# Kernel optimization log

Measured on AMD Instinct MI355X. Metric: run time of the kernel, lower is better.

Reference implementation:

```python
import jax, jax.numpy as jnp
import numpy as np

KERNEL_MUL = 2.0
KERNEL_NUM = 5


def setup_inputs() -> dict:
    key = jax.random.key(0)
    k1, k2 = jax.random.split(key)
    B, Ns, Nt, K = 4, 2048, 2048, 32
    source = jax.random.normal(k1, (B, Ns, K), dtype=jnp.float32)
    target = jax.random.normal(k2, (B, Nt, K), dtype=jnp.float32)
    return {"source": source, "target": target}


def _mmd_rbf(source, target):
    # source: [B, Ns, K], target: [B, Nt, K]
    Ns = source.shape[1]
    Nt = target.shape[1]
    n_samples = Ns + Nt
    total = jnp.concatenate([source, target], axis=1)  # [B, N, K]
    # Pairwise squared L2 via Gram trick (avoids [B, N, N, K] broadcast tensor)
    sq = jnp.sum(total * total, axis=-1)  # [B, N]
    gram = jnp.einsum('bik,bjk->bij', total, total)  # [B, N, N]
    L2 = sq[:, :, None] + sq[:, None, :] - 2.0 * gram  # [B, N, N]
    # Multi-bandwidth RBF kernel sum
    bw = jnp.sum(L2, axis=(1, 2), keepdims=True) / (n_samples ** 2 - n_samples + 1e-8)  # [B,1,1]
    bw = bw / (KERNEL_MUL ** (KERNEL_NUM // 2))
    # Small fixed loop over bandwidths; accumulate to avoid [K_num, B, N, N] stack.
    kernel = jnp.zeros_like(L2)
    for i in range(KERNEL_NUM):
        kernel = kernel + jnp.exp(-L2 / (bw * (KERNEL_MUL ** i)) + 1e-8)
    # Quadrant means
    N = Ns
    XX = kernel[:, :N, :N].mean(axis=(1, 2))
    YY = kernel[:, N:, N:].mean(axis=(1, 2))
    XY = kernel[:, :N, N:].mean(axis=(1, 2))
    YX = kernel[:, N:, :N].mean(axis=(1, 2))
    return XX + YY - XY - YX  # [B]


def reference(source, target):
    return _mmd_rbf(source, target)
```

## Files before the change

### kernel.cpp

```cpp
#include <hip/hip_runtime.h>
#include <hip/hip_bf16.h>


#define NPTS 4096
#define HALF 2048
#define KDIM 32
#define T3   128
#define NTB3 32
#define NPAIR3 528
#define GRIDX 128
#define SPREAD 64

#define WS_SQ    0
#define WS_PART  65536
#define WS_QUAD  82432
#define WS_COEF  90640
#define WS_FRAG  98304
#define WS_NEED  (98304 + 4 * NPTS * 128)

typedef __attribute__((ext_vector_type(8))) short short8v;
typedef __attribute__((ext_vector_type(4))) float f32x4;

__device__ __forceinline__ float fast_exp2(float x) {
#if __has_builtin(__builtin_amdgcn_exp2f)
  return __builtin_amdgcn_exp2f(x);
#else
  return exp2f(x);
#endif
}

__device__ __forceinline__ unsigned int bf16_rne(float x) {
  unsigned int u = __float_as_uint(x);
  return (u + 0x7fffu + ((u >> 16) & 1u)) >> 16;
}

__device__ __forceinline__ const float* point_ptr(const float* __restrict__ src,
                                                  const float* __restrict__ tgt,
                                                  int b, int p) {
  return (p < HALF) ? src + ((size_t)b * HALF + p) * KDIM
                    : tgt + ((size_t)b * HALF + (p - HALF)) * KDIM;
}

__global__ void mmd_pass1(const float* __restrict__ src, const float* __restrict__ tgt,
                          float* __restrict__ sqArr, double* __restrict__ part1,
                          double* __restrict__ quadbuf,
                          unsigned char* __restrict__ frags, int preFlag) {
  const int b = blockIdx.y;
  const int p = blockIdx.x * 256 + threadIdx.x;

  if (blockIdx.x == 0)
    quadbuf[b * 4 * SPREAD + threadIdx.x] = 0.0;

  const float* __restrict__ xp = point_ptr(src, tgt, b, p);
  float x[KDIM];
#pragma unroll
  for (int q = 0; q < 8; ++q) {
    float4 v = reinterpret_cast<const float4*>(xp)[q];
    x[4*q+0] = v.x; x[4*q+1] = v.y; x[4*q+2] = v.z; x[4*q+3] = v.w;
  }
  float s0 = 0.f, s1 = 0.f, s2 = 0.f, s3 = 0.f;
#pragma unroll
  for (int q = 0; q < 8; ++q) {
    s0 = fmaf(x[4*q+0], x[4*q+0], s0);
    s1 = fmaf(x[4*q+1], x[4*q+1], s1);
    s2 = fmaf(x[4*q+2], x[4*q+2], s2);
    s3 = fmaf(x[4*q+3], x[4*q+3], s3);
  }
  float sq = (s0 + s1) + (s2 + s3);
  sqArr[(size_t)b * NPTS + p] = sq;

  if (preFlag) {
    unsigned int hw[16], lw[16];
#pragma unroll
    for (int e = 0; e < 16; ++e) {
      const float xa = x[2*e], xb = x[2*e+1];
      const unsigned int ha = bf16_rne(xa);
      const unsigned int la = bf16_rne(xa - __uint_as_float(ha << 16));
      const unsigned int hb = bf16_rne(xb);
      const unsigned int lb = bf16_rne(xb - __uint_as_float(hb << 16));
      hw[e] = ha | (hb << 16);
      lw[e] = la | (lb << 16);
    }
    uint4* dst = reinterpret_cast<uint4*>(frags + (size_t)(b * NPTS + p) * 128);
#pragma unroll
    for (int c = 0; c < 4; ++c)
      dst[c] = make_uint4(hw[4*c], hw[4*c+1], hw[4*c+2], hw[4*c+3]);
#pragma unroll
    for (int c = 0; c < 4; ++c)
      dst[4 + c] = make_uint4(lw[4*c], lw[4*c+1], lw[4*c+2], lw[4*c+3]);
  }

  __shared__ float lx[256][KDIM + 1];
  __shared__ float part[8][KDIM];
  __shared__ float sqpart[4];

#pragma unroll
  for (int k = 0; k < KDIM; ++k) lx[threadIdx.x][k] = x[k];

  float w = sq;
#pragma unroll
  for (int off = 32; off > 0; off >>= 1) w += __shfl_down(w, off, 64);
  if ((threadIdx.x & 63) == 0) sqpart[threadIdx.x >> 6] = w;
  __syncthreads();

  const int k = threadIdx.x & 31, g = threadIdx.x >> 5;
  float ps = 0.f;
#pragma unroll 8
  for (int r = 0; r < 32; ++r) ps += lx[g * 32 + r][k];
  part[g][k] = ps;
  __syncthreads();

  double* slot = part1 + ((size_t)b * 16 + blockIdx.x) * 33;
  if (threadIdx.x < 32) {
    float tot = 0.f;
#pragma unroll
    for (int gg = 0; gg < 8; ++gg) tot += part[gg][threadIdx.x];
    slot[1 + threadIdx.x] = (double)tot;
  }
  if (threadIdx.x == 63)
    slot[0] = (double)(sqpart[0] + sqpart[1] + sqpart[2] + sqpart[3]);
}

__global__ void mmd_pass2(const double* __restrict__ part1, float* __restrict__ coef) {
  const int b = threadIdx.x >> 6;
  const int lane = threadIdx.x & 63;
  __shared__ double red[4][33];
  if (lane < 33) {
    double s = 0.0;
    for (int blk = 0; blk < 16; ++blk) s += part1[((size_t)b * 16 + blk) * 33 + lane];
    red[b][lane] = s;
  }
  __syncthreads();
  if (lane == 0) {
    double ssq = red[b][0], s2 = 0.0;
    for (int k = 1; k <= 32; ++k) s2 += red[b][k] * red[b][k];
    const double N = (double)NPTS;
    double bw = (2.0 * N * ssq - 2.0 * s2) / (N * N - N + 1e-8);
    bw *= 0.25;
    coef[b] = (float)(-1.4426950408889634 / (bw * 16.0));
  }
}

__device__ __forceinline__ short8v lds_frag(const unsigned char* base, int p,
                                            int half, int lk) {
  const int slot = (half * 4 + lk) ^ (p & 7);
  return *reinterpret_cast<const short8v*>(base + p * 128 + slot * 16);
}

template <bool PRE>
__global__ void __launch_bounds__(512, 4)
mmd_pass3(const float* __restrict__ src, const float* __restrict__ tgt,
          const float* __restrict__ sqArr, const float* __restrict__ coef,
          const unsigned char* __restrict__ frags,
          double* __restrict__ quadbuf) {
  const int bid = blockIdx.x;
  const int b = blockIdx.y;
  const int tid = threadIdx.x;
  const int lane = tid & 63;
  const int w = tid >> 6;
  const int lm = lane & 15;
  const int lk = lane >> 4;
  const int wr = w & 3;
  const int wc = w >> 2;

  __shared__ __align__(16) unsigned char fragA[2][T3 * 128];
  __shared__ __align__(16) unsigned char fragB[2][T3 * 128];
  __shared__ __align__(16) float s_sqA[2][T3];
  __shared__ __align__(16) float s_sqB[2][T3];
  __shared__ double wsum[2][8];

  const float nc4 = coef[b];
  const float m2nc = -2.0f * nc4;
  const float* __restrict__ sqG = sqArr + (size_t)b * NPTS;
  const uint4* __restrict__ gfr =
      reinterpret_cast<const uint4*>(frags) + (size_t)b * NPTS * 8;

  const int npair = (bid + 4 * GRIDX < NPAIR3) ? 5 : 4;

  int bxA[5], byA[5];
#pragma unroll
  for (int it = 0; it < 5; ++it) {
    const int pi = bid + it * GRIDX;
    int y = (int)((sqrtf((float)(8 * pi + 1)) - 1.0f) * 0.5f);
    while ((y + 1) * (y + 2) / 2 <= pi) ++y;
    while (y * (y + 1) / 2 > pi) --y;
    byA[it] = y; bxA[it] = pi - y * (y + 1) / 2;
  }

  {
    const int bx = bxA[0], by = byA[0];
    if constexpr (PRE) {
#pragma unroll
      for (int i = 0; i < 2; ++i) {
        const int g = tid + i * 512;
        const int p = g >> 3, s = g & 7;
        const int d = p * 8 + (s ^ (p & 7));
        reinterpret_cast<uint4*>(fragA[0])[d] = gfr[(size_t)bx * 1024 + g];
        reinterpret_cast<uint4*>(fragB[0])[d] = gfr[(size_t)by * 1024 + g];
      }
    } else {
      if (tid < 256) {
        const int pt = tid & 127;
        const bool isB = tid >= 128;
        const float* fp = point_ptr(src, tgt, b, (isB ? by : bx) * T3 + pt);
        unsigned int hw[16], lw[16];
#pragma unroll
        for (int e = 0; e < 16; ++e) {
          const float xa = fp[2*e], xb = fp[2*e+1];
          const unsigned int ha = bf16_rne(xa);
          const unsigned int la = bf16_rne(xa - __uint_as_float(ha << 16));
          const unsigned int hb = bf16_rne(xb);
          const unsigned int lb = bf16_rne(xb - __uint_as_float(hb << 16));
          hw[e] = ha | (hb << 16);
          lw[e] = la | (lb << 16);
        }
        uint4* dst = reinterpret_cast<uint4*>((isB ? fragB[0] : fragA[0]) + pt * 128);
#pragma unroll
        for (int s = 0; s < 8; ++s) {
          const unsigned int* s4 = (s < 4) ? &hw[s * 4] : &lw[(s - 4) * 4];
          dst[s ^ (pt & 7)] = make_uint4(s4[0], s4[1], s4[2], s4[3]);
        }
      }
    }
    if (tid < 128) s_sqA[0][tid] = sqG[bx * T3 + tid];
    else if (tid < 256) s_sqB[0][tid - 128] = sqG[by * T3 + (tid - 128)];
  }
  __syncthreads();

  for (int it = 0; it < npair; ++it) {
    const int c = it & 1;
    const int bx = bxA[it], by = byA[it];

    uint4 va[2], vb[2];
    float nsqa = 0.f, nsqb = 0.f;
    const bool havenext = (it + 1 < npair);
    if (havenext) {
      const int nbx = bxA[it + 1], nby = byA[it + 1];
      if constexpr (PRE) {
#pragma unroll
        for (int i = 0; i < 2; ++i) {
          const int g = tid + i * 512;
          va[i] = gfr[(size_t)nbx * 1024 + g];
          vb[i] = gfr[(size_t)nby * 1024 + g];
        }
      }
      if (tid < 128) nsqa = sqG[nbx * T3 + tid];
      else if (tid < 256) nsqb = sqG[nby * T3 + (tid - 128)];
    }

    const unsigned char* fA = fragA[c];
    const unsigned char* fB = fragB[c];

    short8v Bh[4], Bl[4];
    float sjn[4];
#pragma unroll
    for (int cg = 0; cg < 4; ++cg) {
      const int p = wc * 64 + cg * 16 + lm;
      Bh[cg] = lds_frag(fB, p, 0, lk);
      Bl[cg] = lds_frag(fB, p, 1, lk);
      sjn[cg] = s_sqB[c][p] * nc4;
    }

    double accd = 0.0;
#pragma unroll
    for (int rg = 0; rg < 2; ++rg) {
      const int pa = wr * 32 + rg * 16 + lm;
      const short8v Ah = lds_frag(fA, pa, 0, lk);
      const short8v Al = lds_frag(fA, pa, 1, lk);
      const float4 sqi4 = *reinterpret_cast<const float4*>(
          &s_sqA[c][wr * 32 + rg * 16 + lk * 4]);
      const float sin_[4] = {sqi4.x * nc4, sqi4.y * nc4, sqi4.z * nc4, sqi4.w * nc4};
#pragma unroll
      for (int cg = 0; cg < 4; ++cg) {
        f32x4 accP = {0.f, 0.f, 0.f, 0.f};
        f32x4 accQ = {0.f, 0.f, 0.f, 0.f};
        accP = __builtin_amdgcn_mfma_f32_16x16x32_bf16(Ah, Bh[cg], accP, 0, 0, 0);
        accQ = __builtin_amdgcn_mfma_f32_16x16x32_bf16(Ah, Bl[cg], accQ, 0, 0, 0);
        accP = __builtin_amdgcn_mfma_f32_16x16x32_bf16(Al, Bl[cg], accP, 0, 0, 0);
        accQ = __builtin_amdgcn_mfma_f32_16x16x32_bf16(Al, Bh[cg], accQ, 0, 0, 0);
        float rs = 0.f;
#pragma unroll
        for (int reg = 0; reg < 4; ++reg) {
          const float dot = accP[reg] + accQ[reg];
          const float arg = fmaf(dot, m2nc, sin_[reg] + sjn[cg]);
          float e = fast_exp2(arg);
          float s = e;
          e *= e; s += e;
          e *= e; s += e;
          e *= e; s += e;
          e *= e; s += e;
          rs += s;
        }
        accd += (double)rs;
      }
    }

#pragma unroll
    for (int off = 32; off > 0; off >>= 1) accd += __shfl_down(accd, off, 64);
    if (lane == 0) wsum[c][w] = accd;

    if (havenext) {
      if constexpr (PRE) {
#pragma unroll
        for (int i = 0; i < 2; ++i) {
          const int g = tid + i * 512;
          const int p = g >> 3, s = g & 7;
          const int d = p * 8 + (s ^ (p & 7));
          reinterpret_cast<uint4*>(fragA[c ^ 1])[d] = va[i];
          reinterpret_cast<uint4*>(fragB[c ^ 1])[d] = vb[i];
        }
      } else {
        const int nbx = bxA[it + 1], nby = byA[it + 1];
        if (tid < 256) {
          const int pt = tid & 127;
          const bool isB = tid >= 128;
          const float* fp = point_ptr(src, tgt, b, (isB ? nby : nbx) * T3 + pt);
          unsigned int hw[16], lw[16];
#pragma unroll
          for (int e = 0; e < 16; ++e) {
            const float xa = fp[2*e], xb = fp[2*e+1];
            const unsigned int ha = bf16_rne(xa);
            const unsigned int la = bf16_rne(xa - __uint_as_float(ha << 16));
            const unsigned int hb = bf16_rne(xb);
            const unsigned int lb = bf16_rne(xb - __uint_as_float(hb << 16));
            hw[e] = ha | (hb << 16);
            lw[e] = la | (lb << 16);
          }
          uint4* dst = reinterpret_cast<uint4*>(
              (isB ? fragB[c ^ 1] : fragA[c ^ 1]) + pt * 128);
#pragma unroll
          for (int s = 0; s < 8; ++s) {
            const unsigned int* s4 = (s < 4) ? &hw[s * 4] : &lw[(s - 4) * 4];
            dst[s ^ (pt & 7)] = make_uint4(s4[0], s4[1], s4[2], s4[3]);
          }
        }
      }
      if (tid < 128) s_sqA[c ^ 1][tid] = nsqa;
      else if (tid < 256) s_sqB[c ^ 1][tid - 128] = nsqb;
    }

    __syncthreads();

    if (tid == 0) {
      double tot = 0.0;
#pragma unroll
      for (int ww = 0; ww < 8; ++ww) tot += wsum[c][ww];
      const int rh = (bx >= NTB3 / 2) ? 1 : 0;
      const int ch = (by >= NTB3 / 2) ? 1 : 0;
      const int q  = (rh << 1) | ch;
      const int qT = (ch << 1) | rh;
      const int slot = (bx + by * NTB3) & (SPREAD - 1);
      atomicAdd(&quadbuf[(((b << 2) | q) * SPREAD) + slot], tot);
      if (bx != by)
        atomicAdd(&quadbuf[(((b << 2) | qT) * SPREAD) + slot], tot);
    }
  }
}

__global__ void mmd_pass4(const double* __restrict__ quadbuf, float* __restrict__ out) {
  const int tid = threadIdx.x;
  const int qq = tid >> 6, i = tid & 63;
  __shared__ double wsum[4];
  const double inv = 1.0 / ((double)HALF * (double)HALF);
  for (int b = 0; b < 4; ++b) {
    double v = quadbuf[((b << 2) | qq) * SPREAD + i];
    double sv = (qq == 0 || qq == 3) ? v : -v;
#pragma unroll
    for (int off = 32; off > 0; off >>= 1) sv += __shfl_down(sv, off, 64);
    if ((tid & 63) == 0) wsum[qq] = sv;
    __syncthreads();
    if (tid == 0) out[b] = (float)((wsum[0] + wsum[1] + wsum[2] + wsum[3]) * inv);
    __syncthreads();
  }
}

extern "C" void kernel_launch(void* const* d_in, const int* in_sizes, int n_in,
                              void* d_out, int out_size, void* d_ws, size_t ws_size,
                              hipStream_t stream) {
  const float* src = (const float*)d_in[0];
  const float* tgt = (const float*)d_in[1];
  float* out = (float*)d_out;

  char* ws = (char*)d_ws;
  float*         sqArr   = (float*)(ws + WS_SQ);
  double*        part1   = (double*)(ws + WS_PART);
  double*        quadbuf = (double*)(ws + WS_QUAD);
  float*         coef    = (float*)(ws + WS_COEF);
  unsigned char* frags   = (unsigned char*)(ws + WS_FRAG);

  const int pre = (ws_size >= (size_t)WS_NEED) ? 1 : 0;

  mmd_pass1<<<dim3(NPTS / 256, 4), 256, 0, stream>>>(src, tgt, sqArr, part1,
                                                     quadbuf, frags, pre);
  mmd_pass2<<<1, 256, 0, stream>>>(part1, coef);
  if (pre)
    mmd_pass3<true><<<dim3(GRIDX, 4), 512, 0, stream>>>(src, tgt, sqArr, coef,
                                                        frags, quadbuf);
  else
    mmd_pass3<false><<<dim3(GRIDX, 4), 512, 0, stream>>>(src, tgt, sqArr, coef,
                                                         frags, quadbuf);
  mmd_pass4<<<1, 256, 0, stream>>>(quadbuf, out);
}
```

Baseline: 95.36 us.

## Fuse bandwidth reduction into pair kernel, single-buffer tiles, widen grid

Removes the separate single-block pass2 kernel: each pass3 block now reduces the per-block partial sums itself to compute the RBF coefficient, saving one launch. Pass1 uses 64-thread blocks so part1 has 64 slices per batch. Pass3 grows to 176 blocks per batch (3 tile pairs each, 528 total), drops the double-buffered LDS prefetch in favour of a single buffer with a sync, and raises launch bounds to 6 blocks per CU. Less LDS and more blocks aim to raise occupancy and spread the work, at the cost of exposed load latency between tiles and redundant coefficient reduction in every block.

```diff
diff --git a/kernel.cpp b/kernel.cpp
--- a/kernel.cpp
+++ b/kernel.cpp
@@ -8,15 +8,14 @@
 #define T3   128
 #define NTB3 32
 #define NPAIR3 528
-#define GRIDX 128
+#define GRIDX 176
 #define SPREAD 64
 
 #define WS_SQ    0
 #define WS_PART  65536
-#define WS_QUAD  82432
-#define WS_COEF  90640
-#define WS_FRAG  98304
-#define WS_NEED  (98304 + 4 * NPTS * 128)
+#define WS_QUAD  133120
+#define WS_FRAG  147456
+#define WS_NEED  (147456 + 4 * NPTS * 128)
 
 typedef __attribute__((ext_vector_type(8))) short short8v;
 typedef __attribute__((ext_vector_type(4))) float f32x4;
@@ -41,15 +40,20 @@
                     : tgt + ((size_t)b * HALF + (p - HALF)) * KDIM;
 }
 
-__global__ void mmd_pass1(const float* __restrict__ src, const float* __restrict__ tgt,
-                          float* __restrict__ sqArr, double* __restrict__ part1,
-                          double* __restrict__ quadbuf,
-                          unsigned char* __restrict__ frags, int preFlag) {
+__global__ void __launch_bounds__(64)
+mmd_pass1(const float* __restrict__ src, const float* __restrict__ tgt,
+          float* __restrict__ sqArr, double* __restrict__ part1,
+          double* __restrict__ quadbuf,
+          unsigned char* __restrict__ frags, int preFlag) {
   const int b = blockIdx.y;
-  const int p = blockIdx.x * 256 + threadIdx.x;
-
-  if (blockIdx.x == 0)
-    quadbuf[b * 4 * SPREAD + threadIdx.x] = 0.0;
+  const int tid = threadIdx.x;
+  const int p = blockIdx.x * 64 + tid;
+
+  if (blockIdx.x == 0) {
+#pragma unroll
+    for (int i = 0; i < 4; ++i)
+      quadbuf[b * 4 * SPREAD + i * 64 + tid] = 0.0;
+  }
 
   const float* __restrict__ xp = point_ptr(src, tgt, b, p);
   float x[KDIM];
@@ -66,7 +70,7 @@
     s2 = fmaf(x[4*q+2], x[4*q+2], s2);
     s3 = fmaf(x[4*q+3], x[4*q+3], s3);
   }
-  float sq = (s0 + s1) + (s2 + s3);
+  const float sq = (s0 + s1) + (s2 + s3);
   sqArr[(size_t)b * NPTS + p] = sq;
 
   if (preFlag) {
@@ -90,55 +94,22 @@
       dst[4 + c] = make_uint4(lw[4*c], lw[4*c+1], lw[4*c+2], lw[4*c+3]);
   }
 
-  __shared__ float lx[256][KDIM + 1];
-  __shared__ float part[8][KDIM];
-  __shared__ float sqpart[4];
-
-#pragma unroll
-  for (int k = 0; k < KDIM; ++k) lx[threadIdx.x][k] = x[k];
-
+  __shared__ float lx[64][KDIM + 1];
+#pragma unroll
+  for (int k = 0; k < KDIM; ++k) lx[tid][k] = x[k];
+  __syncthreads();
+
+  double* slot = part1 + ((size_t)b * 64 + blockIdx.x) * 33;
+  if (tid < 32) {
+    float ps = 0.f;
+#pragma unroll 16
+    for (int r = 0; r < 64; ++r) ps += lx[r][tid];
+    slot[1 + tid] = (double)ps;
+  }
   float w = sq;
 #pragma unroll
   for (int off = 32; off > 0; off >>= 1) w += __shfl_down(w, off, 64);
-  if ((threadIdx.x & 63) == 0) sqpart[threadIdx.x >> 6] = w;
-  __syncthreads();
-
-  const int k = threadIdx.x & 31, g = threadIdx.x >> 5;
-  float ps = 0.f;
-#pragma unroll 8
-  for (int r = 0; r < 32; ++r) ps += lx[g * 32 + r][k];
-  part[g][k] = ps;
-  __syncthreads();
-
-  double* slot = part1 + ((size_t)b * 16 + blockIdx.x) * 33;
-  if (threadIdx.x < 32) {
-    float tot = 0.f;
-#pragma unroll
-    for (int gg = 0; gg < 8; ++gg) tot += part[gg][threadIdx.x];
-    slot[1 + threadIdx.x] = (double)tot;
-  }
-  if (threadIdx.x == 63)
-    slot[0] = (double)(sqpart[0] + sqpart[1] + sqpart[2] + sqpart[3]);
-}
-
-__global__ void mmd_pass2(const double* __restrict__ part1, float* __restrict__ coef) {
-  const int b = threadIdx.x >> 6;
-  const int lane = threadIdx.x & 63;
-  __shared__ double red[4][33];
-  if (lane < 33) {
-    double s = 0.0;
-    for (int blk = 0; blk < 16; ++blk) s += part1[((size_t)b * 16 + blk) * 33 + lane];
-    red[b][lane] = s;
-  }
-  __syncthreads();
-  if (lane == 0) {
-    double ssq = red[b][0], s2 = 0.0;
-    for (int k = 1; k <= 32; ++k) s2 += red[b][k] * red[b][k];
-    const double N = (double)NPTS;
-    double bw = (2.0 * N * ssq - 2.0 * s2) / (N * N - N + 1e-8);
-    bw *= 0.25;
-    coef[b] = (float)(-1.4426950408889634 / (bw * 16.0));
-  }
+  if (tid == 0) slot[0] = (double)w;
 }
 
 __device__ __forceinline__ short8v lds_frag(const unsigned char* base, int p,
@@ -148,9 +119,9 @@
 }
 
 template <bool PRE>
-__global__ void __launch_bounds__(512, 4)
+__global__ void __launch_bounds__(512, 6)
 mmd_pass3(const float* __restrict__ src, const float* __restrict__ tgt,
-          const float* __restrict__ sqArr, const float* __restrict__ coef,
+          const float* __restrict__ sqArr, const double* __restrict__ part1,
           const unsigned char* __restrict__ frags,
           double* __restrict__ quadbuf) {
   const int bid = blockIdx.x;
@@ -163,23 +134,37 @@
   const int wr = w & 3;
   const int wc = w >> 2;
 
-  __shared__ __align__(16) unsigned char fragA[2][T3 * 128];
-  __shared__ __align__(16) unsigned char fragB[2][T3 * 128];
-  __shared__ __align__(16) float s_sqA[2][T3];
-  __shared__ __align__(16) float s_sqB[2][T3];
-  __shared__ double wsum[2][8];
-
-  const float nc4 = coef[b];
-  const float m2nc = -2.0f * nc4;
+  __shared__ __align__(16) unsigned char fragA[T3 * 128];
+  __shared__ __align__(16) unsigned char fragB[T3 * 128];
+  __shared__ float s_sqA[T3], s_sqB[T3];
+  __shared__ double red[33];
+  __shared__ float s_nc4;
+  __shared__ double wsum[8];
+
   const float* __restrict__ sqG = sqArr + (size_t)b * NPTS;
   const uint4* __restrict__ gfr =
       reinterpret_cast<const uint4*>(frags) + (size_t)b * NPTS * 8;
 
-  const int npair = (bid + 4 * GRIDX < NPAIR3) ? 5 : 4;
-
-  int bxA[5], byA[5];
-#pragma unroll
-  for (int it = 0; it < 5; ++it) {
+  if (tid < 33) {
+    double s = 0.0;
+#pragma unroll 16
+    for (int blk = 0; blk < 64; ++blk)
+      s += part1[((size_t)b * 64 + blk) * 33 + tid];
+    red[tid] = s;
+  }
+  __syncthreads();
+  if (tid == 0) {
+    double ssq = red[0], s2 = 0.0;
+    for (int k = 1; k <= 32; ++k) s2 += red[k] * red[k];
+    const double N = (double)NPTS;
+    double bw = (2.0 * N * ssq - 2.0 * s2) / (N * N - N + 1e-8);
+    bw *= 0.25;
+    s_nc4 = (float)(-1.4426950408889634 / (bw * 16.0));
+  }
+
+  int bxA[3], byA[3];
+#pragma unroll
+  for (int it = 0; it < 3; ++it) {
     const int pi = bid + it * GRIDX;
     int y = (int)((sqrtf((float)(8 * pi + 1)) - 1.0f) * 0.5f);
     while ((y + 1) * (y + 2) / 2 <= pi) ++y;
@@ -195,14 +180,116 @@
         const int g = tid + i * 512;
         const int p = g >> 3, s = g & 7;
         const int d = p * 8 + (s ^ (p & 7));
-        reinterpret_cast<uint4*>(fragA[0])[d] = gfr[(size_t)bx * 1024 + g];
-        reinterpret_cast<uint4*>(fragB[0])[d] = gfr[(size_t)by * 1024 + g];
-      }
-    } else {
-      if (tid < 256) {
+        reinterpret_cast<uint4*>(fragA)[d] = gfr[(size_t)bx * 1024 + g];
+        reinterpret_cast<uint4*>(fragB)[d] = gfr[(size_t)by * 1024 + g];
+      }
+    } else if (tid < 256) {
+      const int pt = tid & 127;
+      const bool isB = tid >= 128;
+      const float* fp = point_ptr(src, tgt, b, (isB ? by : bx) * T3 + pt);
+      unsigned int hw[16], lw[16];
+#pragma unroll
+      for (int e = 0; e < 16; ++e) {
+        const float xa = fp[2*e], xb = fp[2*e+1];
+        const unsigned int ha = bf16_rne(xa);
+        const unsigned int la = bf16_rne(xa - __uint_as_float(ha << 16));
+        const unsigned int hb = bf16_rne(xb);
+        const unsigned int lb = bf16_rne(xb - __uint_as_float(hb << 16));
+        hw[e] = ha | (hb << 16);
+        lw[e] = la | (lb << 16);
+      }
+      uint4* dst = reinterpret_cast<uint4*>((isB ? fragB : fragA) + pt * 128);
+#pragma unroll
+      for (int s = 0; s < 8; ++s) {
+        const unsigned int* s4 = (s < 4) ? &hw[s * 4] : &lw[(s - 4) * 4];
+        dst[s ^ (pt & 7)] = make_uint4(s4[0], s4[1], s4[2], s4[3]);
+      }
+    }
+    if (tid < 128) s_sqA[tid] = sqG[bx * T3 + tid];
+    else if (tid < 256) s_sqB[tid - 128] = sqG[by * T3 + (tid - 128)];
+  }
+  __syncthreads();
+
+  const float nc4 = s_nc4;
+  const float m2nc = -2.0f * nc4;
+
+  for (int it = 0; it < 3; ++it) {
+    const int bx = bxA[it], by = byA[it];
+
+    double accd = 0.0;
+#pragma unroll
+    for (int cg = 0; cg < 4; ++cg) {
+      const int pb = wc * 64 + cg * 16 + lm;
+      const short8v Bh = lds_frag(fragB, pb, 0, lk);
+      const short8v Bl = lds_frag(fragB, pb, 1, lk);
+      const float sjn = s_sqB[pb] * nc4;
+#pragma unroll
+      for (int rg = 0; rg < 2; ++rg) {
+        const int pa = wr * 32 + rg * 16 + lm;
+        const short8v Ah = lds_frag(fragA, pa, 0, lk);
+        const short8v Al = lds_frag(fragA, pa, 1, lk);
+        const float4 sqi4 = *reinterpret_cast<const float4*>(
+            &s_sqA[wr * 32 + rg * 16 + lk * 4]);
+        const float sin_[4] = {sqi4.x * nc4, sqi4.y * nc4,
+                               sqi4.z * nc4, sqi4.w * nc4};
+        f32x4 accP = {0.f, 0.f, 0.f, 0.f};
+        f32x4 accQ = {0.f, 0.f, 0.f, 0.f};
+        accP = __builtin_amdgcn_mfma_f32_16x16x32_bf16(Ah, Bh, accP, 0, 0, 0);
+        accQ = __builtin_amdgcn_mfma_f32_16x16x32_bf16(Ah, Bl, accQ, 0, 0, 0);
+        accP = __builtin_amdgcn_mfma_f32_16x16x32_bf16(Al, Bl, accP, 0, 0, 0);
+        accQ = __builtin_amdgcn_mfma_f32_16x16x32_bf16(Al, Bh, accQ, 0, 0, 0);
+        float rs = 0.f;
+#pragma unroll
+        for (int reg = 0; reg < 4; ++reg) {
+          const float dot = accP[reg] + accQ[reg];
+          const float arg = fmaf(dot, m2nc, sin_[reg] + sjn);
+          float e = fast_exp2(arg);
+          float s = e;
+          e *= e; s += e;
+          e *= e; s += e;
+          e *= e; s += e;
+          e *= e; s += e;
+          rs += s;
+        }
+        accd += (double)rs;
+      }
+    }
+
+#pragma unroll
+    for (int off = 32; off > 0; off >>= 1) accd += __shfl_down(accd, off, 64);
+    if (lane == 0) wsum[w] = accd;
+
+    __syncthreads();
+
+    if (tid == 0) {
+      double tot = 0.0;
+#pragma unroll
+      for (int ww = 0; ww < 8; ++ww) tot += wsum[ww];
+      const int rh = (bx >= NTB3 / 2) ? 1 : 0;
+      const int ch = (by >= NTB3 / 2) ? 1 : 0;
+      const int q  = (rh << 1) | ch;
+      const int qT = (ch << 1) | rh;
+      const int slot = (bx + by * NTB3) & (SPREAD - 1);
+      atomicAdd(&quadbuf[(((b << 2) | q) * SPREAD) + slot], tot);
+      if (bx != by)
+        atomicAdd(&quadbuf[(((b << 2) | qT) * SPREAD) + slot], tot);
+    }
+
+    if (it + 1 < 3) {
+      const int nbx = bxA[it + 1], nby = byA[it + 1];
+      if constexpr (PRE) {
+#pragma unroll
+        for (int i = 0; i < 2; ++i) {
+          const int g = tid + i * 512;
+          const int p = g >> 3, s = g & 7;
+          const int d = p * 8 + (s ^ (p & 7));
+          reinterpret_cast<uint4*>(fragA)[d] = gfr[(size_t)nbx * 1024 + g];
+          reinterpret_cast<uint4*>(fragB)[d] = gfr[(size_t)nby * 1024 + g];
+        }
+      } else if (tid < 256) {
         const int pt = tid & 127;
         const bool isB = tid >= 128;
-        const float* fp = point_ptr(src, tgt, b, (isB ? by : bx) * T3 + pt);
+        const float* fp = point_ptr(src, tgt, b, (isB ? nby : nbx) * T3 + pt);
         unsigned int hw[16], lw[16];
 #pragma unroll
         for (int e = 0; e < 16; ++e) {
@@ -214,145 +301,16 @@
           hw[e] = ha | (hb << 16);
           lw[e] = la | (lb << 16);
         }
-        uint4* dst = reinterpret_cast<uint4*>((isB ? fragB[0] : fragA[0]) + pt * 128);
+        uint4* dst = reinterpret_cast<uint4*>((isB ? fragB : fragA) + pt * 128);
 #pragma unroll
         for (int s = 0; s < 8; ++s) {
           const unsigned int* s4 = (s < 4) ? &hw[s * 4] : &lw[(s - 4) * 4];
           dst[s ^ (pt & 7)] = make_uint4(s4[0], s4[1], s4[2], s4[3]);
         }
       }
-    }
-    if (tid < 128) s_sqA[0][tid] = sqG[bx * T3 + tid];
-    else if (tid < 256) s_sqB[0][tid - 128] = sqG[by * T3 + (tid - 128)];
-  }
-  __syncthreads();
-
-  for (int it = 0; it < npair; ++it) {
-    const int c = it & 1;
-    const int bx = bxA[it], by = byA[it];
-
-    uint4 va[2], vb[2];
-    float nsqa = 0.f, nsqb = 0.f;
-    const bool havenext = (it + 1 < npair);
-    if (havenext) {
-      const int nbx = bxA[it + 1], nby = byA[it + 1];
-      if constexpr (PRE) {
-#pragma unroll
-        for (int i = 0; i < 2; ++i) {
-          const int g = tid + i * 512;
-          va[i] = gfr[(size_t)nbx * 1024 + g];
-          vb[i] = gfr[(size_t)nby * 1024 + g];
-        }
-      }
-      if (tid < 128) nsqa = sqG[nbx * T3 + tid];
-      else if (tid < 256) nsqb = sqG[nby * T3 + (tid - 128)];
-    }
-
-    const unsigned char* fA = fragA[c];
-    const unsigned char* fB = fragB[c];
-
-    short8v Bh[4], Bl[4];
-    float sjn[4];
-#pragma unroll
-    for (int cg = 0; cg < 4; ++cg) {
-      const int p = wc * 64 + cg * 16 + lm;
-      Bh[cg] = lds_frag(fB, p, 0, lk);
-      Bl[cg] = lds_frag(fB, p, 1, lk);
-      sjn[cg] = s_sqB[c][p] * nc4;
-    }
-
-    double accd = 0.0;
-#pragma unroll
-    for (int rg = 0; rg < 2; ++rg) {
-      const int pa = wr * 32 + rg * 16 + lm;
-      const short8v Ah = lds_frag(fA, pa, 0, lk);
-      const short8v Al = lds_frag(fA, pa, 1, lk);
-      const float4 sqi4 = *reinterpret_cast<const float4*>(
-          &s_sqA[c][wr * 32 + rg * 16 + lk * 4]);
-      const float sin_[4] = {sqi4.x * nc4, sqi4.y * nc4, sqi4.z * nc4, sqi4.w * nc4};
-#pragma unroll
-      for (int cg = 0; cg < 4; ++cg) {
-        f32x4 accP = {0.f, 0.f, 0.f, 0.f};
-        f32x4 accQ = {0.f, 0.f, 0.f, 0.f};
-        accP = __builtin_amdgcn_mfma_f32_16x16x32_bf16(Ah, Bh[cg], accP, 0, 0, 0);
-        accQ = __builtin_amdgcn_mfma_f32_16x16x32_bf16(Ah, Bl[cg], accQ, 0, 0, 0);
-        accP = __builtin_amdgcn_mfma_f32_16x16x32_bf16(Al, Bl[cg], accP, 0, 0, 0);
-        accQ = __builtin_amdgcn_mfma_f32_16x16x32_bf16(Al, Bh[cg], accQ, 0, 0, 0);
-        float rs = 0.f;
-#pragma unroll
-        for (int reg = 0; reg < 4; ++reg) {
-          const float dot = accP[reg] + accQ[reg];
-          const float arg = fmaf(dot, m2nc, sin_[reg] + sjn[cg]);
-          float e = fast_exp2(arg);
-          float s = e;
-          e *= e; s += e;
-          e *= e; s += e;
-          e *= e; s += e;
-          e *= e; s += e;
-          rs += s;
-        }
-        accd += (double)rs;
-      }
-    }
-
-#pragma unroll
-    for (int off = 32; off > 0; off >>= 1) accd += __shfl_down(accd, off, 64);
-    if (lane == 0) wsum[c][w] = accd;
-
-    if (havenext) {
-      if constexpr (PRE) {
-#pragma unroll
-        for (int i = 0; i < 2; ++i) {
-          const int g = tid + i * 512;
-          const int p = g >> 3, s = g & 7;
-          const int d = p * 8 + (s ^ (p & 7));
-          reinterpret_cast<uint4*>(fragA[c ^ 1])[d] = va[i];
-          reinterpret_cast<uint4*>(fragB[c ^ 1])[d] = vb[i];
-        }
-      } else {
-        const int nbx = bxA[it + 1], nby = byA[it + 1];
-        if (tid < 256) {
-          const int pt = tid & 127;
-          const bool isB = tid >= 128;
-          const float* fp = point_ptr(src, tgt, b, (isB ? nby : nbx) * T3 + pt);
-          unsigned int hw[16], lw[16];
-#pragma unroll
-          for (int e = 0; e < 16; ++e) {
-            const float xa = fp[2*e], xb = fp[2*e+1];
-            const unsigned int ha = bf16_rne(xa);
-            const unsigned int la = bf16_rne(xa - __uint_as_float(ha << 16));
-            const unsigned int hb = bf16_rne(xb);
-            const unsigned int lb = bf16_rne(xb - __uint_as_float(hb << 16));
-            hw[e] = ha | (hb << 16);
-            lw[e] = la | (lb << 16);
-          }
-          uint4* dst = reinterpret_cast<uint4*>(
-              (isB ? fragB[c ^ 1] : fragA[c ^ 1]) + pt * 128);
-#pragma unroll
-          for (int s = 0; s < 8; ++s) {
-            const unsigned int* s4 = (s < 4) ? &hw[s * 4] : &lw[(s - 4) * 4];
-            dst[s ^ (pt & 7)] = make_uint4(s4[0], s4[1], s4[2], s4[3]);
-          }
-        }
-      }
-      if (tid < 128) s_sqA[c ^ 1][tid] = nsqa;
-      else if (tid < 256) s_sqB[c ^ 1][tid - 128] = nsqb;
-    }
-
-    __syncthreads();
-
-    if (tid == 0) {
-      double tot = 0.0;
-#pragma unroll
-      for (int ww = 0; ww < 8; ++ww) tot += wsum[c][ww];
-      const int rh = (bx >= NTB3 / 2) ? 1 : 0;
-      const int ch = (by >= NTB3 / 2) ? 1 : 0;
-      const int q  = (rh << 1) | ch;
-      const int qT = (ch << 1) | rh;
-      const int slot = (bx + by * NTB3) & (SPREAD - 1);
-      atomicAdd(&quadbuf[(((b << 2) | q) * SPREAD) + slot], tot);
-      if (bx != by)
-        atomicAdd(&quadbuf[(((b << 2) | qT) * SPREAD) + slot], tot);
+      if (tid < 128) s_sqA[tid] = sqG[nbx * T3 + tid];
+      else if (tid < 256) s_sqB[tid - 128] = sqG[nby * T3 + (tid - 128)];
+      __syncthreads();
     }
   }
 }
@@ -385,19 +343,17 @@
   float*         sqArr   = (float*)(ws + WS_SQ);
   double*        part1   = (double*)(ws + WS_PART);
   double*        quadbuf = (double*)(ws + WS_QUAD);
-  float*         coef    = (float*)(ws + WS_COEF);
   unsigned char* frags   = (unsigned char*)(ws + WS_FRAG);
 
   const int pre = (ws_size >= (size_t)WS_NEED) ? 1 : 0;
 
-  mmd_pass1<<<dim3(NPTS / 256, 4), 256, 0, stream>>>(src, tgt, sqArr, part1,
-                                                     quadbuf, frags, pre);
-  mmd_pass2<<<1, 256, 0, stream>>>(part1, coef);
+  mmd_pass1<<<dim3(64, 4), 64, 0, stream>>>(src, tgt, sqArr, part1,
+                                            quadbuf, frags, pre);
   if (pre)
-    mmd_pass3<true><<<dim3(GRIDX, 4), 512, 0, stream>>>(src, tgt, sqArr, coef,
+    mmd_pass3<true><<<dim3(GRIDX, 4), 512, 0, stream>>>(src, tgt, sqArr, part1,
                                                         frags, quadbuf);
   else
-    mmd_pass3<false><<<dim3(GRIDX, 4), 512, 0, stream>>>(src, tgt, sqArr, coef,
+    mmd_pass3<false><<<dim3(GRIDX, 4), 512, 0, stream>>>(src, tgt, sqArr, part1,
                                                          frags, quadbuf);
   mmd_pass4<<<1, 256, 0, stream>>>(quadbuf, out);
 }
```

After: 83.75 us. 12.2% less time.
